# Kernel tuning notes

Hardware: AMD Instinct MI355X
Metric: run time of the kernel (lower is better)

Reference implementation:

```python
import jax, jax.numpy as jnp
import numpy as np

EPS = 1e-12
B, C, L, A = 8, 256, 8192, 128


def setup_inputs() -> dict:
    key = jax.random.key(0)
    ks = jax.random.split(key, 6)
    x = jax.random.normal(ks[0], (B, C, L), dtype=jnp.float32)
    # fraction of valid frames per utterance, kept >= 0.5 so mask is never empty
    lengths = jax.random.uniform(ks[1], (B,), dtype=jnp.float32, minval=0.5, maxval=1.0)
    def init_w(k, shape, fan_in):
        return jax.random.normal(k, shape, dtype=jnp.float32) / np.sqrt(fan_in).astype(np.float32)
    w_val = init_w(ks[2], (C, 3 * C), 3 * C)      # values_layer: Linear(3C -> C)
    b_val = jnp.zeros((C,), jnp.float32)
    w_tdnn = init_w(ks[3], (A, 3 * C), 3 * C)     # TDNNBlock conv1x1: 3C -> A
    b_tdnn = jnp.zeros((A,), jnp.float32)
    bn_gamma = jnp.ones((A,), jnp.float32)        # BatchNorm affine (eval: running stats folded)
    bn_beta = jnp.zeros((A,), jnp.float32)
    w_conv = init_w(ks[4], (C, A), A)             # score conv1x1: A -> C
    b_conv = jnp.zeros((C,), jnp.float32)
    return {"x": x, "lengths": lengths, "w_val": w_val, "b_val": b_val,
            "w_tdnn": w_tdnn, "b_tdnn": b_tdnn, "bn_gamma": bn_gamma,
            "bn_beta": bn_beta, "w_conv": w_conv, "b_conv": b_conv}


def reference(x, lengths, w_val, b_val, w_tdnn, b_tdnn, bn_gamma, bn_beta, w_conv, b_conv):
    # x: [B, C, L]; lengths: [B] fractions in (0,1]
    Bn, Cn, Ln = x.shape
    mask = (jnp.arange(Ln, dtype=jnp.float32)[None, :] < (lengths * Ln)[:, None]).astype(x.dtype)  # [B, L]
    total = jnp.sum(mask, axis=1, keepdims=True)                     # [B, 1]
    m = (mask / total)[:, None, :]                                   # [B, 1, L]
    # masked global statistics
    gmean = jnp.sum(m * x, axis=2)                                   # [B, C]
    gstd = jnp.sqrt(jnp.clip(jnp.sum(m * (x - gmean[:, :, None]) ** 2, axis=2), EPS))  # [B, C]
    # global context concat -> [B, 3C, L]
    attn = jnp.concatenate([x,
                            jnp.broadcast_to(gmean[:, :, None], (Bn, Cn, Ln)),
                            jnp.broadcast_to(gstd[:, :, None], (Bn, Cn, Ln))], axis=1)
    a = jnp.transpose(attn, (0, 2, 1))                               # [B, L, 3C]
    values = jnp.einsum('blf,cf->blc', a, w_val) + b_val             # [B, L, C]
    # score network: conv1x1 -> ReLU -> BN(affine) -> conv1x1
    h = jax.nn.relu(jnp.einsum('blf,af->bla', a, w_tdnn) + b_tdnn) * bn_gamma + bn_beta  # [B, L, A]
    scores = jnp.einsum('bla,ca->blc', h, w_conv) + b_conv           # [B, L, C]
    neg = jnp.finfo(x.dtype).min
    scores = jnp.where(mask[:, :, None] > 0, scores, neg)
    w = jax.nn.softmax(scores, axis=1)                               # masked softmax over L, per channel
    # attention-weighted mean and variance of values
    amean = jnp.sum(w * values, axis=1)                              # [B, C]
    avar = jnp.sum(w * (values - amean[:, None, :]) ** 2, axis=1)    # [B, C]
    astd = jnp.sqrt(jnp.clip(avar, EPS))
    pooled = jnp.concatenate([amean, astd], axis=-1)[:, None, :]     # [B, 1, 2C]
    return jnp.transpose(pooled, (0, 2, 1))                          # [B, 2C, 1]
```

## Files before the change

### kernel.cpp

```cpp
#include <hip/hip_runtime.h>
#include <float.h>
#include <math.h>

#define B_N 8
#define C_N 256
#define L_N 8192
#define A_N 128
#define LT 64
#define NTILES (L_N / LT)

typedef short bf16x8 __attribute__((ext_vector_type(8)));
typedef float f32x4 __attribute__((ext_vector_type(4)));

__device__ __forceinline__ short f2bf(float f) {
  union { float f; unsigned u; } v; v.f = f;
  unsigned r = v.u + 0x7fffu + ((v.u >> 16) & 1u);
  return (short)(r >> 16);
}

__device__ __forceinline__ unsigned cvt_pk_bf16(float lo, float hi) {
  unsigned r;
  asm("v_cvt_pk_bf16_f32 %0, %1, %2" : "=v"(r) : "v"(lo), "v"(hi));
  return r;
}

__global__ __launch_bounds__(128)
void kA_stats_convert(const float* __restrict__ x, const float* __restrict__ lengths,
                      const float* __restrict__ w_val, const float* __restrict__ w_tdnn,
                      const float* __restrict__ w_conv,
                      float* __restrict__ gmean, float* __restrict__ gstd,
                      short* __restrict__ wv, short* __restrict__ wt, short* __restrict__ wc) {
  if (blockIdx.x < 2048) {
    __shared__ float sm[2][3];
    int blk = blockIdx.x;
    int b = blk >> 8;
    int wave = threadIdx.x >> 6;
    int lane = threadIdx.x & 63;
    float vlen = lengths[b] * (float)L_N;
    const float4* row = (const float4*)(x + (size_t)blk * L_N + wave * (L_N / 2));
    float s = 0.f, s2 = 0.f, cnt = 0.f;
    if (wave == 0) {
#pragma unroll 4
      for (int i = lane; i < 1024; i += 64) {
        float4 q = row[i];
        s += q.x + q.y + q.z + q.w;
        s2 += q.x * q.x + q.y * q.y + q.z * q.z + q.w * q.w;
      }
      cnt = 64.f;
    } else {
      for (int i = lane; i < 1024; i += 64) {
        int l = 4096 + i * 4;
        if ((float)l >= vlen) break;
        float4 q = row[i];
        if ((float)(l + 3) < vlen) {
          s += q.x + q.y + q.z + q.w;
          s2 += q.x * q.x + q.y * q.y + q.z * q.z + q.w * q.w;
          cnt += 4.f;
        } else {
          float e[4] = {q.x, q.y, q.z, q.w};
#pragma unroll
          for (int j = 0; j < 4; ++j) {
            if ((float)(l + j) < vlen) { float t = e[j]; s += t; s2 += t * t; cnt += 1.f; }
          }
        }
      }
    }
#pragma unroll
    for (int off = 32; off; off >>= 1) {
      s += __shfl_xor(s, off); s2 += __shfl_xor(s2, off); cnt += __shfl_xor(cnt, off);
    }
    if (lane == 0) { sm[wave][0] = s; sm[wave][1] = s2; sm[wave][2] = cnt; }
    __syncthreads();
    if (threadIdx.x == 0) {
      float S = sm[0][0] + sm[1][0];
      float S2 = sm[0][1] + sm[1][1];
      float CNT = sm[0][2] + sm[1][2];
      float mean = S / CNT;
      float var = S2 / CNT - mean * mean;
      gmean[blk] = mean;
      gstd[blk] = sqrtf(fmaxf(var, 1e-12f));
    }
  } else {
    int unit = (blockIdx.x - 2048) * 2 + (threadIdx.x >> 6);
    int lane = threadIdx.x & 63;
    int t = unit * 64 + lane;
    const float* src;
    short* dst;
    int p, c, k, rowlen;
    if (t < 16384) {
      p = t * 4;
      int j0 = p & 7, lane_ = (p >> 3) & 63, bi = p >> 9;
      int kblk = bi & 7, colblk = bi >> 3;
      c = colblk * 16 + (lane_ & 15);
      k = kblk * 32 + (lane_ >> 4) * 8 + j0;
      src = w_val; dst = wv; rowlen = 768;
    } else if (t < 24576) {
      p = (t - 16384) * 4;
      int j0 = p & 7, lane_ = (p >> 3) & 63, bi = p >> 9;
      int kblk = bi & 7, colblk = bi >> 3;
      c = colblk * 16 + (lane_ & 15);
      k = kblk * 32 + (lane_ >> 4) * 8 + j0;
      src = w_tdnn; dst = wt; rowlen = 768;
    } else {
      p = (t - 24576) * 4;
      int j0 = p & 7, lane_ = (p >> 3) & 63, bi = p >> 9;
      int kblk = bi & 3, colblk = bi >> 2;
      c = colblk * 16 + (lane_ & 15);
      k = kblk * 32 + (lane_ >> 4) * 8 + j0;
      src = w_conv; dst = wc; rowlen = 128;
    }
    float4 q = *(const float4*)(src + (size_t)c * rowlen + k);
    short4 o = make_short4(f2bf(q.x), f2bf(q.y), f2bf(q.z), f2bf(q.w));
    *(short4*)(dst + p) = o;
  }
}

__global__ __launch_bounds__(256)
void kB_bias(const float* __restrict__ w_val, const float* __restrict__ b_val,
             const float* __restrict__ w_tdnn, const float* __restrict__ b_tdnn,
             const float* __restrict__ gmean, const float* __restrict__ gstd,
             float* __restrict__ bias_val, float* __restrict__ hbias) {
  int unit = blockIdx.x * 4 + (threadIdx.x >> 6);
  int lane = threadIdx.x & 63;
  if (unit < 2048) {
    int b = unit >> 8, c = unit & 255;
    const float* wr = w_val + c * 768;
    const float* gm = gmean + b * 256;
    const float* gs = gstd + b * 256;
    float s = 0.f;
    for (int j = lane; j < 256; j += 64)
      s += gm[j] * wr[256 + j] + gs[j] * wr[512 + j];
#pragma unroll
    for (int off = 32; off; off >>= 1) s += __shfl_xor(s, off);
    if (lane == 0) bias_val[b * 256 + c] = s + b_val[c];
  } else {
    int t = unit - 2048;
    int b = t >> 7, a = t & 127;
    const float* wr = w_tdnn + a * 768;
    const float* gm = gmean + b * 256;
    const float* gs = gstd + b * 256;
    float s = 0.f;
    for (int j = lane; j < 256; j += 64)
      s += gm[j] * wr[256 + j] + gs[j] * wr[512 + j];
#pragma unroll
    for (int off = 32; off; off >>= 1) s += __shfl_xor(s, off);
    if (lane == 0) hbias[b * 128 + a] = s + b_tdnn[a];
  }
}

__global__ __launch_bounds__(512, 4)
void k3_main8w(const float* __restrict__ x, const float* __restrict__ lengths,
               const short* __restrict__ wv, const short* __restrict__ wt,
               const short* __restrict__ wc,
               const float* __restrict__ bias_val, const float* __restrict__ hbias,
               const float* __restrict__ bn_gamma, const float* __restrict__ bn_beta,
               const float* __restrict__ b_conv,
               float4* __restrict__ partial) {
  __shared__ short xs[LT][C_N + 8];
  __shared__ short hs[LT][A_N + 8];

  int blk = blockIdx.x;
  int b = blk >> 7;
  int tile = blk & 127;
  int l0 = tile * LT;
  int tid = threadIdx.x;
  int wave = tid >> 6;
  int lane = tid & 63;
  int lr = lane & 15;
  int lg = lane >> 4;

  float vlen = lengths[b] * (float)L_N;

  if ((float)l0 >= vlen) {
    if (lg == 0) {
#pragma unroll
      for (int nt = 0; nt < 2; ++nt) {
        int c = wave * 32 + nt * 16 + lr;
        partial[(size_t)((b * NTILES + tile) * C_N) + c] = make_float4(-FLT_MAX, 0.f, 0.f, 0.f);
      }
    }
    return;
  }

  int ai = wave * 16 + lr;
  float hb = hbias[b * A_N + ai];
  float g  = bn_gamma[ai];
  float be = bn_beta[ai];
  float bc2[2], bv2[2];
#pragma unroll
  for (int nt = 0; nt < 2; ++nt) {
    int c = wave * 32 + nt * 16 + lr;
    bc2[nt] = b_conv[c];
    bv2[nt] = bias_val[b * C_N + c];
  }

  {
    int lgrp = tid & 15;
    int crow = tid >> 4;
    const float* xb = x + (size_t)b * C_N * L_N + l0 + lgrp * 4;
#pragma unroll
    for (int i = 0; i < 2; ++i) {
      int c0 = (i * 32 + crow) * 4;
      float4 q0 = *(const float4*)(xb + (size_t)(c0 + 0) * L_N);
      float4 q1 = *(const float4*)(xb + (size_t)(c0 + 1) * L_N);
      float4 q2 = *(const float4*)(xb + (size_t)(c0 + 2) * L_N);
      float4 q3 = *(const float4*)(xb + (size_t)(c0 + 3) * L_N);
      float e0[4] = {q0.x, q0.y, q0.z, q0.w};
      float e1[4] = {q1.x, q1.y, q1.z, q1.w};
      float e2[4] = {q2.x, q2.y, q2.z, q2.w};
      float e3[4] = {q3.x, q3.y, q3.z, q3.w};
#pragma unroll
      for (int r = 0; r < 4; ++r) {
        unsigned u0 = cvt_pk_bf16(e0[r], e1[r]);
        unsigned u1 = cvt_pk_bf16(e2[r], e3[r]);
        *(uint2*)&xs[lgrp * 4 + r][c0] = make_uint2(u0, u1);
      }
    }
  }
  __syncthreads();

  f32x4 zero4 = {0.f, 0.f, 0.f, 0.f};
  f32x4 accv[4][2];
  f32x4 acch[4];
#pragma unroll
  for (int mt = 0; mt < 4; ++mt) {
#pragma unroll
    for (int nt = 0; nt < 2; ++nt) accv[mt][nt] = zero4;
    acch[mt] = zero4;
  }

  for (int k0 = 0; k0 < C_N; k0 += 32) {
    int kb = k0 >> 5;
    bf16x8 af[4];
#pragma unroll
    for (int mt = 0; mt < 4; ++mt)
      af[mt] = *(const bf16x8*)&xs[mt * 16 + lr][k0 + lg * 8];
#pragma unroll
    for (int nt = 0; nt < 2; ++nt) {
      const bf16x8 bf = *(const bf16x8*)&wv[(((wave * 2 + nt) * 8 + kb) * 64 + lane) * 8];
#pragma unroll
      for (int mt = 0; mt < 4; ++mt)
        accv[mt][nt] = __builtin_amdgcn_mfma_f32_16x16x32_bf16(af[mt], bf, accv[mt][nt], 0, 0, 0);
    }
    {
      const bf16x8 bf = *(const bf16x8*)&wt[((wave * 8 + kb) * 64 + lane) * 8];
#pragma unroll
      for (int mt = 0; mt < 4; ++mt)
        acch[mt] = __builtin_amdgcn_mfma_f32_16x16x32_bf16(af[mt], bf, acch[mt], 0, 0, 0);
    }
  }
  __builtin_amdgcn_sched_barrier(0);

#pragma unroll
  for (int mt = 0; mt < 4; ++mt) {
#pragma unroll
    for (int r = 0; r < 4; ++r) {
      float hv = acch[mt][r] + hb;
      hv = fmaxf(hv, 0.f) * g + be;
      hs[mt * 16 + lg * 4 + r][ai] = f2bf(hv);
    }
  }
  __syncthreads();

  f32x4 accs[4][2];
#pragma unroll
  for (int mt = 0; mt < 4; ++mt)
#pragma unroll
    for (int nt = 0; nt < 2; ++nt) accs[mt][nt] = zero4;

  for (int k0 = 0; k0 < A_N; k0 += 32) {
    int kb = k0 >> 5;
    bf16x8 af[4];
#pragma unroll
    for (int mt = 0; mt < 4; ++mt)
      af[mt] = *(const bf16x8*)&hs[mt * 16 + lr][k0 + lg * 8];
#pragma unroll
    for (int nt = 0; nt < 2; ++nt) {
      const bf16x8 bf = *(const bf16x8*)&wc[(((wave * 2 + nt) * 4 + kb) * 64 + lane) * 8];
#pragma unroll
      for (int mt = 0; mt < 4; ++mt)
        accs[mt][nt] = __builtin_amdgcn_mfma_f32_16x16x32_bf16(af[mt], bf, accs[mt][nt], 0, 0, 0);
    }
  }
  __builtin_amdgcn_sched_barrier(0);

  bool fullvalid = (float)(l0 + LT - 1) < vlen;

#pragma unroll
  for (int nt = 0; nt < 2; ++nt) {
    int c = wave * 32 + nt * 16 + lr;
    float bc = bc2[nt];
    float bv = bv2[nt];
    float m = -FLT_MAX, ss = 0.f, sv = 0.f, svv = 0.f;
    if (fullvalid) {
#pragma unroll
      for (int mt = 0; mt < 4; ++mt)
#pragma unroll
        for (int r = 0; r < 4; ++r) m = fmaxf(m, accs[mt][nt][r]);
      m = fmaxf(m, __shfl_xor(m, 16));
      m = fmaxf(m, __shfl_xor(m, 32));
#pragma unroll
      for (int mt = 0; mt < 4; ++mt) {
#pragma unroll
        for (int r = 0; r < 4; ++r) {
          float p = __expf(accs[mt][nt][r] - m);
          float v = accv[mt][nt][r] + bv;
          ss += p; sv += p * v; svv += p * v * v;
        }
      }
    } else {
      float lbase = (float)(l0 + lg * 4);
#pragma unroll
      for (int mt = 0; mt < 4; ++mt)
#pragma unroll
        for (int r = 0; r < 4; ++r) {
          bool valid = (lbase + (float)(mt * 16 + r)) < vlen;
          m = fmaxf(m, valid ? accs[mt][nt][r] : -FLT_MAX);
        }
      m = fmaxf(m, __shfl_xor(m, 16));
      m = fmaxf(m, __shfl_xor(m, 32));
#pragma unroll
      for (int mt = 0; mt < 4; ++mt) {
#pragma unroll
        for (int r = 0; r < 4; ++r) {
          bool valid = (lbase + (float)(mt * 16 + r)) < vlen;
          float p = valid ? __expf(accs[mt][nt][r] - m) : 0.f;
          float v = accv[mt][nt][r] + bv;
          ss += p; sv += p * v; svv += p * v * v;
        }
      }
    }
    m += bc;
    ss += __shfl_xor(ss, 16); ss += __shfl_xor(ss, 32);
    sv += __shfl_xor(sv, 16); sv += __shfl_xor(sv, 32);
    svv += __shfl_xor(svv, 16); svv += __shfl_xor(svv, 32);
    if (lg == 0) {
      partial[(size_t)((b * NTILES + tile) * C_N) + c] = make_float4(m, ss, sv, svv);
    }
  }
}

__global__ __launch_bounds__(64)
void k4_combine(const float4* __restrict__ partial, float* __restrict__ out) {
  int blk = blockIdx.x;
  int b = blk >> 8, c = blk & 255;
  int lane = threadIdx.x;
  float m = -FLT_MAX, s = 0.f, sv = 0.f, svv = 0.f;
  for (int t = lane; t < NTILES; t += 64) {
    float4 q = partial[(size_t)((b * NTILES + t) * C_N) + c];
    float M = fmaxf(m, q.x);
    float e1 = __expf(m - M), e2 = __expf(q.x - M);
    s = s * e1 + q.y * e2;
    sv = sv * e1 + q.z * e2;
    svv = svv * e1 + q.w * e2;
    m = M;
  }
#pragma unroll
  for (int off = 32; off; off >>= 1) {
    float m2 = __shfl_xor(m, off), s2 = __shfl_xor(s, off);
    float sv2 = __shfl_xor(sv, off), svv2 = __shfl_xor(svv, off);
    float M = fmaxf(m, m2);
    float e1 = __expf(m - M), e2 = __expf(m2 - M);
    s = s * e1 + s2 * e2;
    sv = sv * e1 + sv2 * e2;
    svv = svv * e1 + svv2 * e2;
    m = M;
  }
  if (lane == 0) {
    float amean = sv / s;
    float avar = svv / s - amean * amean;
    out[b * 512 + c] = amean;
    out[b * 512 + 256 + c] = sqrtf(fmaxf(avar, 1e-12f));
  }
}

extern "C" void kernel_launch(void* const* d_in, const int* in_sizes, int n_in,
                              void* d_out, int out_size, void* d_ws, size_t ws_size,
                              hipStream_t stream) {
  const float* x        = (const float*)d_in[0];
  const float* lengths  = (const float*)d_in[1];
  const float* w_val    = (const float*)d_in[2];
  const float* b_val    = (const float*)d_in[3];
  const float* w_tdnn   = (const float*)d_in[4];
  const float* b_tdnn   = (const float*)d_in[5];
  const float* bn_gamma = (const float*)d_in[6];
  const float* bn_beta  = (const float*)d_in[7];
  const float* w_conv   = (const float*)d_in[8];
  const float* b_conv   = (const float*)d_in[9];
  float* out = (float*)d_out;

  char* ws = (char*)d_ws;
  float* gmean     = (float*)(ws + 0);
  float* gstd      = (float*)(ws + 8 * 1024);
  float* bias_val  = (float*)(ws + 16 * 1024);
  float* hbias     = (float*)(ws + 24 * 1024);
  short* wv        = (short*)(ws + 32 * 1024);
  short* wt        = (short*)(ws + 160 * 1024);
  short* wc        = (short*)(ws + 224 * 1024);
  float4* partial  = (float4*)(ws + 512 * 1024);

  kA_stats_convert<<<dim3(2304), dim3(128), 0, stream>>>(x, lengths, w_val, w_tdnn, w_conv,
                                                         gmean, gstd, wv, wt, wc);
  kB_bias<<<dim3(768), dim3(256), 0, stream>>>(w_val, b_val, w_tdnn, b_tdnn,
                                               gmean, gstd, bias_val, hbias);
  k3_main8w<<<dim3(B_N * NTILES), dim3(512), 0, stream>>>(x, lengths, wv, wt, wc,
                                                          bias_val, hbias, bn_gamma, bn_beta,
                                                          b_conv, partial);
  k4_combine<<<dim3(B_N * C_N), dim3(64), 0, stream>>>(partial, out);
}
```

Measured before the change: 47.68 us.

## Process two L-tiles per block with register prefetch of next x tile

```diff
diff --git a/kernel.cpp b/kernel.cpp
--- a/kernel.cpp
+++ b/kernel.cpp
@@ -160,27 +160,30 @@
   __shared__ short hs[LT][A_N + 8];
 
   int blk = blockIdx.x;
-  int b = blk >> 7;
-  int tile = blk & 127;
-  int l0 = tile * LT;
+  int b = blk >> 6;
+  int t0 = (blk & 63) * 2;
   int tid = threadIdx.x;
   int wave = tid >> 6;
   int lane = tid & 63;
   int lr = lane & 15;
   int lg = lane >> 4;
+  int lgrp = tid & 15;
+  int crow = tid >> 4;
 
   float vlen = lengths[b] * (float)L_N;
 
-  if ((float)l0 >= vlen) {
+  if ((float)(t0 * LT) >= vlen) {
     if (lg == 0) {
 #pragma unroll
       for (int nt = 0; nt < 2; ++nt) {
         int c = wave * 32 + nt * 16 + lr;
-        partial[(size_t)((b * NTILES + tile) * C_N) + c] = make_float4(-FLT_MAX, 0.f, 0.f, 0.f);
+        partial[(size_t)((b * NTILES + t0) * C_N) + c]     = make_float4(-FLT_MAX, 0.f, 0.f, 0.f);
+        partial[(size_t)((b * NTILES + t0 + 1) * C_N) + c] = make_float4(-FLT_MAX, 0.f, 0.f, 0.f);
       }
     }
     return;
   }
+  bool t1_valid = (float)((t0 + 1) * LT) < vlen;
 
   int ai = wave * 16 + lr;
   float hb = hbias[b * A_N + ai];
@@ -195,9 +198,7 @@
   }
 
   {
-    int lgrp = tid & 15;
-    int crow = tid >> 4;
-    const float* xb = x + (size_t)b * C_N * L_N + l0 + lgrp * 4;
+    const float* xb = x + (size_t)b * C_N * L_N + t0 * LT + lgrp * 4;
 #pragma unroll
     for (int i = 0; i < 2; ++i) {
       int c0 = (i * 32 + crow) * 4;
@@ -220,122 +221,168 @@
   __syncthreads();
 
   f32x4 zero4 = {0.f, 0.f, 0.f, 0.f};
-  f32x4 accv[4][2];
-  f32x4 acch[4];
-#pragma unroll
-  for (int mt = 0; mt < 4; ++mt) {
-#pragma unroll
-    for (int nt = 0; nt < 2; ++nt) accv[mt][nt] = zero4;
-    acch[mt] = zero4;
-  }
-
-  for (int k0 = 0; k0 < C_N; k0 += 32) {
-    int kb = k0 >> 5;
-    bf16x8 af[4];
+
+#pragma unroll 1
+  for (int ti = 0; ti < 2; ++ti) {
+    int tile = t0 + ti;
+    int l0 = tile * LT;
+
+    f32x4 accv[4][2];
+    f32x4 acch[4];
+#pragma unroll
+    for (int mt = 0; mt < 4; ++mt) {
+#pragma unroll
+      for (int nt = 0; nt < 2; ++nt) accv[mt][nt] = zero4;
+      acch[mt] = zero4;
+    }
+
+    for (int k0 = 0; k0 < C_N; k0 += 32) {
+      int kb = k0 >> 5;
+      bf16x8 af[4];
+#pragma unroll
+      for (int mt = 0; mt < 4; ++mt)
+        af[mt] = *(const bf16x8*)&xs[mt * 16 + lr][k0 + lg * 8];
+#pragma unroll
+      for (int nt = 0; nt < 2; ++nt) {
+        const bf16x8 bf = *(const bf16x8*)&wv[(((wave * 2 + nt) * 8 + kb) * 64 + lane) * 8];
+#pragma unroll
+        for (int mt = 0; mt < 4; ++mt)
+          accv[mt][nt] = __builtin_amdgcn_mfma_f32_16x16x32_bf16(af[mt], bf, accv[mt][nt], 0, 0, 0);
+      }
+      {
+        const bf16x8 bf = *(const bf16x8*)&wt[((wave * 8 + kb) * 64 + lane) * 8];
+#pragma unroll
+        for (int mt = 0; mt < 4; ++mt)
+          acch[mt] = __builtin_amdgcn_mfma_f32_16x16x32_bf16(af[mt], bf, acch[mt], 0, 0, 0);
+      }
+    }
+    __builtin_amdgcn_sched_barrier(0);
+
+    bool pf = (ti == 0) && t1_valid;
+    float4 q[8];
+    if (pf) {
+      const float* xb = x + (size_t)b * C_N * L_N + (t0 + 1) * LT + lgrp * 4;
+#pragma unroll
+      for (int i = 0; i < 2; ++i)
+#pragma unroll
+        for (int j = 0; j < 4; ++j)
+          q[i * 4 + j] = *(const float4*)(xb + (size_t)((i * 32 + crow) * 4 + j) * L_N);
+    }
+
+#pragma unroll
+    for (int mt = 0; mt < 4; ++mt) {
+#pragma unroll
+      for (int r = 0; r < 4; ++r) {
+        float hv = acch[mt][r] + hb;
+        hv = fmaxf(hv, 0.f) * g + be;
+        hs[mt * 16 + lg * 4 + r][ai] = f2bf(hv);
+      }
+    }
+    __syncthreads();
+
+    f32x4 accs[4][2];
 #pragma unroll
     for (int mt = 0; mt < 4; ++mt)
-      af[mt] = *(const bf16x8*)&xs[mt * 16 + lr][k0 + lg * 8];
+#pragma unroll
+      for (int nt = 0; nt < 2; ++nt) accs[mt][nt] = zero4;
+
+    for (int k0 = 0; k0 < A_N; k0 += 32) {
+      int kb = k0 >> 5;
+      bf16x8 af[4];
+#pragma unroll
+      for (int mt = 0; mt < 4; ++mt)
+        af[mt] = *(const bf16x8*)&hs[mt * 16 + lr][k0 + lg * 8];
+#pragma unroll
+      for (int nt = 0; nt < 2; ++nt) {
+        const bf16x8 bf = *(const bf16x8*)&wc[(((wave * 2 + nt) * 4 + kb) * 64 + lane) * 8];
+#pragma unroll
+        for (int mt = 0; mt < 4; ++mt)
+          accs[mt][nt] = __builtin_amdgcn_mfma_f32_16x16x32_bf16(af[mt], bf, accs[mt][nt], 0, 0, 0);
+      }
+    }
+    __builtin_amdgcn_sched_barrier(0);
+
+    bool fullvalid = (float)(l0 + LT - 1) < vlen;
+
 #pragma unroll
     for (int nt = 0; nt < 2; ++nt) {
-      const bf16x8 bf = *(const bf16x8*)&wv[(((wave * 2 + nt) * 8 + kb) * 64 + lane) * 8];
-#pragma unroll
-      for (int mt = 0; mt < 4; ++mt)
-        accv[mt][nt] = __builtin_amdgcn_mfma_f32_16x16x32_bf16(af[mt], bf, accv[mt][nt], 0, 0, 0);
-    }
-    {
-      const bf16x8 bf = *(const bf16x8*)&wt[((wave * 8 + kb) * 64 + lane) * 8];
-#pragma unroll
-      for (int mt = 0; mt < 4; ++mt)
-        acch[mt] = __builtin_amdgcn_mfma_f32_16x16x32_bf16(af[mt], bf, acch[mt], 0, 0, 0);
-    }
-  }
-  __builtin_amdgcn_sched_barrier(0);
-
-#pragma unroll
-  for (int mt = 0; mt < 4; ++mt) {
-#pragma unroll
-    for (int r = 0; r < 4; ++r) {
-      float hv = acch[mt][r] + hb;
-      hv = fmaxf(hv, 0.f) * g + be;
-      hs[mt * 16 + lg * 4 + r][ai] = f2bf(hv);
-    }
-  }
-  __syncthreads();
-
-  f32x4 accs[4][2];
-#pragma unroll
-  for (int mt = 0; mt < 4; ++mt)
-#pragma unroll
-    for (int nt = 0; nt < 2; ++nt) accs[mt][nt] = zero4;
-
-  for (int k0 = 0; k0 < A_N; k0 += 32) {
-    int kb = k0 >> 5;
-    bf16x8 af[4];
-#pragma unroll
-    for (int mt = 0; mt < 4; ++mt)
-      af[mt] = *(const bf16x8*)&hs[mt * 16 + lr][k0 + lg * 8];
-#pragma unroll
-    for (int nt = 0; nt < 2; ++nt) {
-      const bf16x8 bf = *(const bf16x8*)&wc[(((wave * 2 + nt) * 4 + kb) * 64 + lane) * 8];
-#pragma unroll
-      for (int mt = 0; mt < 4; ++mt)
-        accs[mt][nt] = __builtin_amdgcn_mfma_f32_16x16x32_bf16(af[mt], bf, accs[mt][nt], 0, 0, 0);
-    }
-  }
-  __builtin_amdgcn_sched_barrier(0);
-
-  bool fullvalid = (float)(l0 + LT - 1) < vlen;
-
-#pragma unroll
-  for (int nt = 0; nt < 2; ++nt) {
-    int c = wave * 32 + nt * 16 + lr;
-    float bc = bc2[nt];
-    float bv = bv2[nt];
-    float m = -FLT_MAX, ss = 0.f, sv = 0.f, svv = 0.f;
-    if (fullvalid) {
-#pragma unroll
-      for (int mt = 0; mt < 4; ++mt)
-#pragma unroll
-        for (int r = 0; r < 4; ++r) m = fmaxf(m, accs[mt][nt][r]);
-      m = fmaxf(m, __shfl_xor(m, 16));
-      m = fmaxf(m, __shfl_xor(m, 32));
-#pragma unroll
-      for (int mt = 0; mt < 4; ++mt) {
+      int c = wave * 32 + nt * 16 + lr;
+      float bc = bc2[nt];
+      float bv = bv2[nt];
+      float m = -FLT_MAX, ss = 0.f, sv = 0.f, svv = 0.f;
+      if (fullvalid) {
+#pragma unroll
+        for (int mt = 0; mt < 4; ++mt)
+#pragma unroll
+          for (int r = 0; r < 4; ++r) m = fmaxf(m, accs[mt][nt][r]);
+        m = fmaxf(m, __shfl_xor(m, 16));
+        m = fmaxf(m, __shfl_xor(m, 32));
+#pragma unroll
+        for (int mt = 0; mt < 4; ++mt) {
+#pragma unroll
+          for (int r = 0; r < 4; ++r) {
+            float p = __expf(accs[mt][nt][r] - m);
+            float v = accv[mt][nt][r] + bv;
+            ss += p; sv += p * v; svv += p * v * v;
+          }
+        }
+      } else {
+        float lbase = (float)(l0 + lg * 4);
+#pragma unroll
+        for (int mt = 0; mt < 4; ++mt)
+#pragma unroll
+          for (int r = 0; r < 4; ++r) {
+            bool valid = (lbase + (float)(mt * 16 + r)) < vlen;
+            m = fmaxf(m, valid ? accs[mt][nt][r] : -FLT_MAX);
+          }
+        m = fmaxf(m, __shfl_xor(m, 16));
+        m = fmaxf(m, __shfl_xor(m, 32));
+#pragma unroll
+        for (int mt = 0; mt < 4; ++mt) {
+#pragma unroll
+          for (int r = 0; r < 4; ++r) {
+            bool valid = (lbase + (float)(mt * 16 + r)) < vlen;
+            float p = valid ? __expf(accs[mt][nt][r] - m) : 0.f;
+            float v = accv[mt][nt][r] + bv;
+            ss += p; sv += p * v; svv += p * v * v;
+          }
+        }
+      }
+      m += bc;
+      ss += __shfl_xor(ss, 16); ss += __shfl_xor(ss, 32);
+      sv += __shfl_xor(sv, 16); sv += __shfl_xor(sv, 32);
+      svv += __shfl_xor(svv, 16); svv += __shfl_xor(svv, 32);
+      if (lg == 0) {
+        partial[(size_t)((b * NTILES + tile) * C_N) + c] = make_float4(m, ss, sv, svv);
+      }
+    }
+
+    if (ti == 0) {
+      if (!t1_valid) {
+        if (lg == 0) {
+#pragma unroll
+          for (int nt = 0; nt < 2; ++nt) {
+            int c = wave * 32 + nt * 16 + lr;
+            partial[(size_t)((b * NTILES + t0 + 1) * C_N) + c] = make_float4(-FLT_MAX, 0.f, 0.f, 0.f);
+          }
+        }
+        return;
+      }
+#pragma unroll
+      for (int i = 0; i < 2; ++i) {
+        int c0 = (i * 32 + crow) * 4;
+        float e0[4] = {q[i*4+0].x, q[i*4+0].y, q[i*4+0].z, q[i*4+0].w};
+        float e1[4] = {q[i*4+1].x, q[i*4+1].y, q[i*4+1].z, q[i*4+1].w};
+        float e2[4] = {q[i*4+2].x, q[i*4+2].y, q[i*4+2].z, q[i*4+2].w};
+        float e3[4] = {q[i*4+3].x, q[i*4+3].y, q[i*4+3].z, q[i*4+3].w};
 #pragma unroll
         for (int r = 0; r < 4; ++r) {
-          float p = __expf(accs[mt][nt][r] - m);
-          float v = accv[mt][nt][r] + bv;
-          ss += p; sv += p * v; svv += p * v * v;
+          unsigned u0 = cvt_pk_bf16(e0[r], e1[r]);
+          unsigned u1 = cvt_pk_bf16(e2[r], e3[r]);
+          *(uint2*)&xs[lgrp * 4 + r][c0] = make_uint2(u0, u1);
         }
       }
-    } else {
-      float lbase = (float)(l0 + lg * 4);
-#pragma unroll
-      for (int mt = 0; mt < 4; ++mt)
-#pragma unroll
-        for (int r = 0; r < 4; ++r) {
-          bool valid = (lbase + (float)(mt * 16 + r)) < vlen;
-          m = fmaxf(m, valid ? accs[mt][nt][r] : -FLT_MAX);
-        }
-      m = fmaxf(m, __shfl_xor(m, 16));
-      m = fmaxf(m, __shfl_xor(m, 32));
-#pragma unroll
-      for (int mt = 0; mt < 4; ++mt) {
-#pragma unroll
-        for (int r = 0; r < 4; ++r) {
-          bool valid = (lbase + (float)(mt * 16 + r)) < vlen;
-          float p = valid ? __expf(accs[mt][nt][r] - m) : 0.f;
-          float v = accv[mt][nt][r] + bv;
-          ss += p; sv += p * v; svv += p * v * v;
-        }
-      }
-    }
-    m += bc;
-    ss += __shfl_xor(ss, 16); ss += __shfl_xor(ss, 32);
-    sv += __shfl_xor(sv, 16); sv += __shfl_xor(sv, 32);
-    svv += __shfl_xor(svv, 16); svv += __shfl_xor(svv, 32);
-    if (lg == 0) {
-      partial[(size_t)((b * NTILES + tile) * C_N) + c] = make_float4(m, ss, sv, svv);
+      __syncthreads();
     }
   }
 }
@@ -403,8 +450,8 @@
                                                          gmean, gstd, wv, wt, wc);
   kB_bias<<<dim3(768), dim3(256), 0, stream>>>(w_val, b_val, w_tdnn, b_tdnn,
                                                gmean, gstd, bias_val, hbias);
-  k3_main8w<<<dim3(B_N * NTILES), dim3(512), 0, stream>>>(x, lengths, wv, wt, wc,
-                                                          bias_val, hbias, bn_gamma, bn_beta,
-                                                          b_conv, partial);
+  k3_main8w<<<dim3(B_N * NTILES / 2), dim3(512), 0, stream>>>(x, lengths, wv, wt, wc,
+                                                              bias_val, hbias, bn_gamma, bn_beta,
+                                                              b_conv, partial);
   k4_combine<<<dim3(B_N * C_N), dim3(64), 0, stream>>>(partial, out);
 }
```

Result: slower. 98.16 us, median of 2 (+105.9%).
